# Kernel tuning notes

Hardware: AMD Instinct MI355X
Metric: run time of the kernel (lower is better)

Reference implementation:

```python
import jax, jax.numpy as jnp
import numpy as np

B, T, V, E, H = 256, 512, 30000, 256, 32


def _run_dir(x, mask, Wih, Whh, bih, bhh, reverse):
    # x: [B,T,D], mask: [B,T] bool. PyTorch GRU gate order: r, z, n.
    gi = jnp.einsum('btd,gd->btg', x, Wih) + bih  # precompute input gates [B,T,3H]
    h0 = jnp.zeros((x.shape[0], Whh.shape[1]), x.dtype)

    def step(h, inp):
        gi_t, m_t = inp
        gh = h @ Whh.T + bhh
        ir, iz, inn = jnp.split(gi_t, 3, axis=-1)
        hr, hz, hn = jnp.split(gh, 3, axis=-1)
        r = jax.nn.sigmoid(ir + hr)
        z = jax.nn.sigmoid(iz + hz)
        n = jnp.tanh(inn + r * hn)
        h_new = (1.0 - z) * n + z * h
        # packed-sequence semantics: freeze state at padded steps
        h = jnp.where(m_t[:, None], h_new, h)
        return h, h

    hT, ys = jax.lax.scan(step, h0, (jnp.swapaxes(gi, 0, 1), mask.T), reverse=reverse)
    return jnp.swapaxes(ys, 0, 1), hT  # outputs [B,T,H], final hidden [B,H]


def _bigru_layer(x, mask, pf, pb):
    of, hf = _run_dir(x, mask, *pf, reverse=False)
    ob, hb = _run_dir(x, mask, *pb, reverse=True)
    return jnp.concatenate([of, ob], axis=-1), hf, hb


def setup_inputs() -> dict:
    key = jax.random.key(0)
    ks = jax.random.split(key, 24)
    lengths = jax.random.randint(ks[0], (B,), 1, T + 1)
    mask = (jnp.arange(T)[None, :] < lengths[:, None]).astype(jnp.int32)
    ids = jax.random.randint(ks[1], (B, T), 1, V)
    ids = jnp.where(mask > 0, ids, 0)  # pad_id = 0 at padded positions
    embed = (jax.random.normal(ks[2], (V, E), jnp.float32) * 0.1).at[0].set(0.0)

    def gru_params(k, din):
        k1, k2, k3, k4 = jax.random.split(k, 4)
        s = 1.0 / np.sqrt(H)
        return (jax.random.uniform(k1, (3 * H, din), jnp.float32, -s, s),
                jax.random.uniform(k2, (3 * H, H), jnp.float32, -s, s),
                jax.random.uniform(k3, (3 * H,), jnp.float32, -s, s),
                jax.random.uniform(k4, (3 * H,), jnp.float32, -s, s))

    inp = {"input_ids": ids, "attention_mask": mask, "embed": embed}
    i = 3
    for layer, din in (("l0", E), ("l1", 2 * H)):
        for d in ("f", "b"):
            Wih, Whh, bih, bhh = gru_params(ks[i], din); i += 1
            inp[f"Wih_{layer}{d}"] = Wih
            inp[f"Whh_{layer}{d}"] = Whh
            inp[f"bih_{layer}{d}"] = bih
            inp[f"bhh_{layer}{d}"] = bhh
    s = 1.0 / np.sqrt(2 * H)
    inp["Wout"] = jax.random.uniform(ks[i], (6, 2 * H), jnp.float32, -s, s)
    inp["bout"] = jax.random.uniform(ks[i + 1], (6,), jnp.float32, -s, s)
    return inp


def reference(input_ids, attention_mask, embed,
              Wih_l0f, Whh_l0f, bih_l0f, bhh_l0f,
              Wih_l0b, Whh_l0b, bih_l0b, bhh_l0b,
              Wih_l1f, Whh_l1f, bih_l1f, bhh_l1f,
              Wih_l1b, Whh_l1b, bih_l1b, bhh_l1b,
              Wout, bout):
    mask = attention_mask > 0
    x = embed[input_ids]  # [B,T,E]
    x1, _, _ = _bigru_layer(x, mask,
                            (Wih_l0f, Whh_l0f, bih_l0f, bhh_l0f),
                            (Wih_l0b, Whh_l0b, bih_l0b, bhh_l0b))
    # no dropout: eval-mode forward
    _, hf, hb = _bigru_layer(x1, mask,
                             (Wih_l1f, Whh_l1f, bih_l1f, bhh_l1f),
                             (Wih_l1b, Whh_l1b, bih_l1b, bhh_l1b))
    top = jnp.concatenate([hf, hb], axis=-1)  # h_n[-2:] -> [B, 2H]
    return top @ Wout.T + bout  # [B, 6]
```

## Files before the change

### kernel.cpp

```cpp
#include <hip/hip_runtime.h>
#include <hip/hip_bf16.h>
#include <stdint.h>

#define B_ 256
#define T_ 512
#define V_ 30000
#define E_ 256
#define H_ 32

typedef float v2f __attribute__((ext_vector_type(2)));
typedef unsigned int uint2e __attribute__((ext_vector_type(2)));

#define LOG2E_F 1.44269504088896340736f

__device__ __forceinline__ float exp2_fast(float x) {
    float r; asm("v_exp_f32 %0, %1" : "=v"(r) : "v"(x)); return r;
}
__device__ __forceinline__ float rcp_fast(float x) {
    float r; asm("v_rcp_f32 %0, %1" : "=v"(r) : "v"(x)); return r;
}
__device__ __forceinline__ void pk_fma(v2f& acc, v2f w, v2f h) {
    asm("v_pk_fma_f32 %0, %1, %2, %0" : "+v"(acc) : "v"(w), "v"(h));
}
template <int CTRL>
__device__ __forceinline__ float mdpp(float x) {
    return __int_as_float(
        __builtin_amdgcn_mov_dpp(__float_as_int(x), CTRL, 0xF, 0xF, true));
}
#define DPP_XOR1  0xB1
#define DPP_XOR2  0x4E
#define DPP_XOR3  0x1B
#define DPP_XOR7  0x141
#define DPP_XOR15 0x140

__device__ __forceinline__ float swap32(float h) {
    uint2e r = __builtin_amdgcn_permlane32_swap(
        __float_as_uint(h), __float_as_uint(h), false, false);
    return __uint_as_float(r.x ^ r.y ^ __float_as_uint(h));
}

#define GEMM_MT 64
#define GEMM_KC 32
#define GEMM_PA 68
#define GEMM_PB 196

__global__ __launch_bounds__(256) void gemm_gates(
    const float* __restrict__ A, int M, int K,
    const float* __restrict__ Wf, const float* __restrict__ Wb,
    const float* __restrict__ bihf, const float* __restrict__ bhhf,
    const float* __restrict__ bihb, const float* __restrict__ bhhb,
    float* __restrict__ Out)
{
    __shared__ float As[GEMM_KC][GEMM_PA];
    __shared__ float Bs[GEMM_KC][GEMM_PB];

    const int tid = threadIdx.x;
    const int mbase = blockIdx.x * GEMM_MT;
    const int mg = tid >> 5, ng = tid & 31;
    const int m_off = mg * 8, n_off = ng * 6;

    float acc[8][6];
    #pragma unroll
    for (int r = 0; r < 8; ++r)
        #pragma unroll
        for (int c = 0; c < 6; ++c) acc[r][c] = 0.f;

    for (int kc = 0; kc < K; kc += GEMM_KC) {
        #pragma unroll
        for (int i = 0; i < 2; ++i) {
            int fi = tid + 256 * i;
            int row = fi >> 3, cf = fi & 7;
            int m = mbase + row;
            float4 v = make_float4(0.f, 0.f, 0.f, 0.f);
            if (m < M) v = *(const float4*)&A[(size_t)m * K + kc + cf * 4];
            As[cf * 4 + 0][row] = v.x; As[cf * 4 + 1][row] = v.y;
            As[cf * 4 + 2][row] = v.z; As[cf * 4 + 3][row] = v.w;
        }
        #pragma unroll
        for (int i = 0; i < 6; ++i) {
            int fi = tid + 256 * i;
            int g = fi >> 3, cf = fi & 7;
            const float* Wsel = (g < 96) ? (Wf + (size_t)g * K)
                                         : (Wb + (size_t)(g - 96) * K);
            float4 v = *(const float4*)&Wsel[kc + cf * 4];
            Bs[cf * 4 + 0][g] = v.x; Bs[cf * 4 + 1][g] = v.y;
            Bs[cf * 4 + 2][g] = v.z; Bs[cf * 4 + 3][g] = v.w;
        }
        __syncthreads();
        #pragma unroll
        for (int k = 0; k < GEMM_KC; ++k) {
            float a[8], bb[6];
            *(float4*)&a[0] = *(const float4*)&As[k][m_off];
            *(float4*)&a[4] = *(const float4*)&As[k][m_off + 4];
            *(float2*)&bb[0] = *(const float2*)&Bs[k][n_off];
            *(float2*)&bb[2] = *(const float2*)&Bs[k][n_off + 2];
            *(float2*)&bb[4] = *(const float2*)&Bs[k][n_off + 4];
            #pragma unroll
            for (int r = 0; r < 8; ++r)
                #pragma unroll
                for (int c = 0; c < 6; ++c)
                    acc[r][c] = fmaf(a[r], bb[c], acc[r][c]);
        }
        __syncthreads();
    }

    float bias[6], gsc[6];
    #pragma unroll
    for (int c = 0; c < 6; ++c) {
        int g = n_off + c;
        int g96 = (g < 96) ? g : g - 96;
        const float* bih = (g < 96) ? bihf : bihb;
        const float* bhh = (g < 96) ? bhhf : bhhb;
        bias[c] = bih[g96] + ((g96 < 64) ? bhh[g96] : 0.f);
        gsc[c]  = (g96 < 64) ? -LOG2E_F : 2.0f * LOG2E_F;
    }
    #pragma unroll
    for (int r = 0; r < 8; ++r) {
        int m = mbase + m_off + r;
        if (m < M) {
            float* op = &Out[(size_t)m * 192 + n_off];
            #pragma unroll
            for (int c = 0; c < 6; ++c) op[c] = (acc[r][c] + bias[c]) * gsc[c];
        }
    }
}

template <int USE_IDS>
__global__ __launch_bounds__(64, 1) void gru_scan(
    const float* __restrict__ gi,
    const int* __restrict__ ids,
    const int* __restrict__ mask,
    const float* __restrict__ Whh_f, const float* __restrict__ Whh_b,
    const float* __restrict__ bhh_f, const float* __restrict__ bhh_b,
    float* __restrict__ out_seq,
    float* __restrict__ out_fin)
{
    const int l = threadIdx.x;
    const int i16 = l & 15;
    const int row = l >> 4;
    const int hi = (row ^ (row >> 1)) & 1;
    const int j = i16 + 16 * hi;
    const bool lower = l < 32;
    const int dir = blockIdx.x & 1;
    const int b = blockIdx.x >> 1;
    const int bT = b * T_;

    const float* Whh = dir ? Whh_b : Whh_f;
    const float* bhh = dir ? bhh_b : bhh_f;

    const int kA = 16 * hi;
    const int kB = 16 - kA;

    const float sRZ = -LOG2E_F;
    const float sN2 = 2.0f * LOG2E_F;

    const int M0[8] = {0, 2, 7, 5, 15, 13, 8, 10};
    const int M1[8] = {1, 3, 6, 4, 14, 12, 9, 11};

    v2f wAR[8], wAZ[8], wAN[8], wBR[8], wBZ[8], wBN[8];
    #pragma unroll
    for (int q = 0; q < 8; ++q) {
        const int a0 = kA + (i16 ^ M0[q]);
        const int a1 = kA + (i16 ^ M1[q]);
        const int b0 = kB + (i16 ^ M0[q]);
        const int b1 = kB + (i16 ^ M1[q]);
        wAR[q] = (v2f){Whh[j * 32 + a0] * sRZ, Whh[j * 32 + a1] * sRZ};
        wAZ[q] = (v2f){Whh[(32 + j) * 32 + a0] * sRZ, Whh[(32 + j) * 32 + a1] * sRZ};
        wAN[q] = (v2f){Whh[(64 + j) * 32 + a0] * sN2, Whh[(64 + j) * 32 + a1] * sN2};
        wBR[q] = (v2f){Whh[j * 32 + b0] * sRZ, Whh[j * 32 + b1] * sRZ};
        wBZ[q] = (v2f){Whh[(32 + j) * 32 + b0] * sRZ, Whh[(32 + j) * 32 + b1] * sRZ};
        wBN[q] = (v2f){Whh[(64 + j) * 32 + b0] * sN2, Whh[(64 + j) * 32 + b1] * sN2};
    }
    float bns = bhh[64 + j] * sN2;

    #pragma unroll
    for (int q = 0; q < 8; ++q) {
        asm volatile("" : "+v"(wAR[q]), "+v"(wAZ[q]), "+v"(wAN[q]),
                          "+v"(wBR[q]), "+v"(wBZ[q]), "+v"(wBN[q]));
    }
    asm volatile("" : "+v"(bns));

    const int offR = dir * 96 + j;
    const int offZ = dir * 96 + 32 + j;
    const int offN = dir * 96 + 64 + j;

    auto wbase = [&](int c) { return dir ? (bT + 508 - 4 * c) : (bT + 4 * c); };

    int4 ids0 = make_int4(0, 0, 0, 0);
    if (USE_IDS) ids0 = *(const int4*)&ids[wbase(0)];
    int4 mask_use = *(const int4*)&mask[wbase(0)];
    int4 mask_mid = *(const int4*)&mask[wbase(1)];
    int4 mask_in  = make_int4(0, 0, 0, 0);
    int4 ids_pf = make_int4(0, 0, 0, 0), ids_mid = ids_pf, ids_in = ids_pf;
    if (USE_IDS) {
        ids_pf  = *(const int4*)&ids[wbase(1)];
        ids_mid = *(const int4*)&ids[wbase(2)];
    }

    float gR[2][4], gZ[2][4], gN[2][4];
    #pragma unroll
    for (int u = 0; u < 4; ++u) {
        int rowi;
        if (USE_IDS) {
            const int* ip = (const int*)&ids0;
            rowi = dir ? ip[3 - u] : ip[u];
        } else {
            rowi = bT + (dir ? (511 - u) : u);
        }
        const float* gp = gi + (size_t)rowi * 192;
        gR[0][u] = gp[offR];
        gZ[0][u] = gp[offZ];
        gN[0][u] = gp[offN];
    }

    float h = 0.f;

    for (int c2 = 0; c2 < 64; ++c2) {
        #pragma unroll
        for (int pb = 0; pb < 2; ++pb) {
            const int c = 2 * c2 + pb;
            if (USE_IDS) {
                const int ci = (c + 3 < 128) ? (c + 3) : 127;
                ids_in = *(const int4*)&ids[wbase(ci)];
            }
            {
                const int cm = (c + 2 < 128) ? (c + 2) : 127;
                mask_in = *(const int4*)&mask[wbase(cm)];
            }
            const int cN = (c + 1 < 128) ? (c + 1) : 127;

            #pragma unroll
            for (int u = 0; u < 4; ++u) {
                int rowN;
                if (USE_IDS) {
                    const int* ip = (const int*)&ids_pf;
                    rowN = dir ? ip[3 - u] : ip[u];
                } else {
                    rowN = bT + (dir ? (511 - 4 * cN - u) : (4 * cN + u));
                }
                const float* gpN = gi + (size_t)rowN * 192;
                gR[pb ^ 1][u] = gpN[offR];
                gZ[pb ^ 1][u] = gpN[offZ];
                gN[pb ^ 1][u] = gpN[offN];

                const int* mu = (const int*)&mask_use;
                const int m = dir ? mu[3 - u] : mu[u];

                const float hs = swap32(h);

                v2f p[8], p2[8];
                {
                    p[0].x = h;                       p[0].y = mdpp<DPP_XOR1>(h);
                    p[1].x = mdpp<DPP_XOR2>(h);       p[1].y = mdpp<DPP_XOR3>(h);
                    p[2].x = mdpp<DPP_XOR7>(h);       p[2].y = mdpp<DPP_XOR7>(p[0].y);
                    p[3].x = mdpp<DPP_XOR7>(p[1].x);  p[3].y = mdpp<DPP_XOR7>(p[1].y);
                    p[4].x = mdpp<DPP_XOR15>(h);      p[4].y = mdpp<DPP_XOR15>(p[0].y);
                    p[5].x = mdpp<DPP_XOR15>(p[1].x); p[5].y = mdpp<DPP_XOR15>(p[1].y);
                    p[6].x = mdpp<DPP_XOR15>(p[2].x); p[6].y = mdpp<DPP_XOR15>(p[2].y);
                    p[7].x = mdpp<DPP_XOR15>(p[3].x); p[7].y = mdpp<DPP_XOR15>(p[3].y);

                    p2[0].x = hs;                       p2[0].y = mdpp<DPP_XOR1>(hs);
                    p2[1].x = mdpp<DPP_XOR2>(hs);       p2[1].y = mdpp<DPP_XOR3>(hs);
                    p2[2].x = mdpp<DPP_XOR7>(hs);       p2[2].y = mdpp<DPP_XOR7>(p2[0].y);
                    p2[3].x = mdpp<DPP_XOR7>(p2[1].x);  p2[3].y = mdpp<DPP_XOR7>(p2[1].y);
                    p2[4].x = mdpp<DPP_XOR15>(hs);      p2[4].y = mdpp<DPP_XOR15>(p2[0].y);
                    p2[5].x = mdpp<DPP_XOR15>(p2[1].x); p2[5].y = mdpp<DPP_XOR15>(p2[1].y);
                    p2[6].x = mdpp<DPP_XOR15>(p2[2].x); p2[6].y = mdpp<DPP_XOR15>(p2[2].y);
                    p2[7].x = mdpp<DPP_XOR15>(p2[3].x); p2[7].y = mdpp<DPP_XOR15>(p2[3].y);
                }

                v2f aR0 = {0.f, 0.f}, aZ0 = {0.f, 0.f}, aN0 = {0.f, 0.f};
                v2f aR1 = {0.f, 0.f}, aZ1 = {0.f, 0.f}, aN1 = {0.f, 0.f};
                #pragma unroll
                for (int q = 0; q < 8; ++q) {
                    pk_fma(aR0, wAR[q], p[q]);
                    pk_fma(aZ0, wAZ[q], p[q]);
                    pk_fma(aN0, wAN[q], p[q]);
                    pk_fma(aR1, wBR[q], p2[q]);
                    pk_fma(aZ1, wBZ[q], p2[q]);
                    pk_fma(aN1, wBN[q], p2[q]);
                }
                const v2f sR = aR0 + aR1;
                const v2f sZ = aZ0 + aZ1;
                const v2f sN = aN0 + aN1;

                const float yr  = (gR[pb][u] + sR.x) + sR.y;
                const float yz  = (gZ[pb][u] + sZ.x) + sZ.y;
                const float hns = (bns + sN.x) + sN.y;
                const float r = rcp_fast(1.0f + exp2_fast(yr));
                const float z = rcp_fast(1.0f + exp2_fast(yz));
                const float yn = gN[pb][u] + r * hns;
                const float n = fmaf(-2.0f, rcp_fast(1.0f + exp2_fast(yn)), 1.0f);
                const float hnew = n + z * (h - n);
                h = m ? hnew : h;

                if (out_seq != nullptr) {
                    const int t = dir ? (511 - 4 * c - u) : (4 * c + u);
                    if (lower)
                        out_seq[(size_t)(bT + t) * 64 + dir * 32 + j] = h;
                }
            }
            mask_use = mask_mid; mask_mid = mask_in;
            if (USE_IDS) { ids_pf = ids_mid; ids_mid = ids_in; }
        }
    }

    if (out_fin != nullptr && lower)
        out_fin[b * 64 + dir * 32 + j] = h;
}

__global__ void head_kernel(const float* __restrict__ hfin,
                            const float* __restrict__ Wout,
                            const float* __restrict__ bout,
                            float* __restrict__ out)
{
    int idx = blockIdx.x * blockDim.x + threadIdx.x;
    if (idx >= B_ * 6) return;
    int b = idx / 6, o = idx % 6;
    float acc = bout[o];
    const float* hp = hfin + b * 64;
    const float* wp = Wout + o * 64;
    #pragma unroll
    for (int k = 0; k < 64; ++k) acc = fmaf(hp[k], wp[k], acc);
    out[idx] = acc;
}

extern "C" void kernel_launch(void* const* d_in, const int* in_sizes, int n_in,
                              void* d_out, int out_size, void* d_ws, size_t ws_size,
                              hipStream_t stream)
{
    const int*   ids   = (const int*)d_in[0];
    const int*   mask  = (const int*)d_in[1];
    const float* embed = (const float*)d_in[2];
    const float* Wih0f = (const float*)d_in[3];
    const float* Whh0f = (const float*)d_in[4];
    const float* bih0f = (const float*)d_in[5];
    const float* bhh0f = (const float*)d_in[6];
    const float* Wih0b = (const float*)d_in[7];
    const float* Whh0b = (const float*)d_in[8];
    const float* bih0b = (const float*)d_in[9];
    const float* bhh0b = (const float*)d_in[10];
    const float* Wih1f = (const float*)d_in[11];
    const float* Whh1f = (const float*)d_in[12];
    const float* bih1f = (const float*)d_in[13];
    const float* bhh1f = (const float*)d_in[14];
    const float* Wih1b = (const float*)d_in[15];
    const float* Whh1b = (const float*)d_in[16];
    const float* bih1b = (const float*)d_in[17];
    const float* bhh1b = (const float*)d_in[18];
    const float* Wout  = (const float*)d_in[19];
    const float* bout  = (const float*)d_in[20];

    float* ws   = (float*)d_ws;
    float* gbuf = ws;
    float* x1   = ws + (size_t)B_ * T_ * 192;
    float* hfin = x1 + (size_t)B_ * T_ * 64;

    gemm_gates<<<(V_ + GEMM_MT - 1) / GEMM_MT, 256, 0, stream>>>(
        embed, V_, E_, Wih0f, Wih0b, bih0f, bhh0f, bih0b, bhh0b, gbuf);

    gru_scan<1><<<2 * B_, 64, 0, stream>>>(
        gbuf, ids, mask, Whh0f, Whh0b, bhh0f, bhh0b, x1, nullptr);

    gemm_gates<<<(B_ * T_) / GEMM_MT, 256, 0, stream>>>(
        x1, B_ * T_, 64, Wih1f, Wih1b, bih1f, bhh1f, bih1b, bhh1b, gbuf);

    gru_scan<0><<<2 * B_, 64, 0, stream>>>(
        gbuf, nullptr, mask, Whh1f, Whh1b, bhh1f, bhh1b, nullptr, hfin);

    head_kernel<<<(B_ * 6 + 255) / 256, 256, 0, stream>>>(hfin, Wout, bout,
                                                          (float*)d_out);
}
```

Before: 525.4 us.

## Split GRU recurrent matvec across wave halves and reduce partial sums via permlane32

Result: faster. 482.4 us (-8.2%).

```diff
diff --git a/kernel.cpp b/kernel.cpp
--- a/kernel.cpp
+++ b/kernel.cpp
@@ -33,10 +33,15 @@
 #define DPP_XOR7  0x141
 #define DPP_XOR15 0x140
 
-__device__ __forceinline__ float swap32(float h) {
+__device__ __forceinline__ float swap32(float x) {
     uint2e r = __builtin_amdgcn_permlane32_swap(
-        __float_as_uint(h), __float_as_uint(h), false, false);
-    return __uint_as_float(r.x ^ r.y ^ __float_as_uint(h));
+        __float_as_uint(x), __float_as_uint(x), false, false);
+    return __uint_as_float(r.x ^ r.y ^ __float_as_uint(x));
+}
+__device__ __forceinline__ float swap16(float x) {
+    uint2e r = __builtin_amdgcn_permlane16_swap(
+        __float_as_uint(x), __float_as_uint(x), false, false);
+    return __uint_as_float(r.x ^ r.y ^ __float_as_uint(x));
 }
 
 #define GEMM_MT 64
@@ -126,7 +131,9 @@
 }
 
 template <int USE_IDS>
-__global__ __launch_bounds__(64, 1) void gru_scan(
+__global__ __launch_bounds__(64, 1)
+__attribute__((amdgpu_waves_per_eu(1, 1)))
+void gru_scan(
     const float* __restrict__ gi,
     const int* __restrict__ ids,
     const int* __restrict__ mask,
@@ -138,9 +145,11 @@
     const int l = threadIdx.x;
     const int i16 = l & 15;
     const int row = l >> 4;
-    const int hi = (row ^ (row >> 1)) & 1;
+    const int hi = row & 1;
+    const int kh = row >> 1;
     const int j = i16 + 16 * hi;
     const bool lower = l < 32;
+    const bool self_seed = (hi == kh);
     const int dir = blockIdx.x & 1;
     const int b = blockIdx.x >> 1;
     const int bT = b * T_;
@@ -148,36 +157,28 @@
     const float* Whh = dir ? Whh_b : Whh_f;
     const float* bhh = dir ? bhh_b : bhh_f;
 
-    const int kA = 16 * hi;
-    const int kB = 16 - kA;
-
     const float sRZ = -LOG2E_F;
     const float sN2 = 2.0f * LOG2E_F;
 
     const int M0[8] = {0, 2, 7, 5, 15, 13, 8, 10};
     const int M1[8] = {1, 3, 6, 4, 14, 12, 9, 11};
 
-    v2f wAR[8], wAZ[8], wAN[8], wBR[8], wBZ[8], wBN[8];
+    v2f wR[8], wZ[8], wN[8];
     #pragma unroll
     for (int q = 0; q < 8; ++q) {
-        const int a0 = kA + (i16 ^ M0[q]);
-        const int a1 = kA + (i16 ^ M1[q]);
-        const int b0 = kB + (i16 ^ M0[q]);
-        const int b1 = kB + (i16 ^ M1[q]);
-        wAR[q] = (v2f){Whh[j * 32 + a0] * sRZ, Whh[j * 32 + a1] * sRZ};
-        wAZ[q] = (v2f){Whh[(32 + j) * 32 + a0] * sRZ, Whh[(32 + j) * 32 + a1] * sRZ};
-        wAN[q] = (v2f){Whh[(64 + j) * 32 + a0] * sN2, Whh[(64 + j) * 32 + a1] * sN2};
-        wBR[q] = (v2f){Whh[j * 32 + b0] * sRZ, Whh[j * 32 + b1] * sRZ};
-        wBZ[q] = (v2f){Whh[(32 + j) * 32 + b0] * sRZ, Whh[(32 + j) * 32 + b1] * sRZ};
-        wBN[q] = (v2f){Whh[(64 + j) * 32 + b0] * sN2, Whh[(64 + j) * 32 + b1] * sN2};
+        const int c0 = kh * 16 + (i16 ^ M0[q]);
+        const int c1 = kh * 16 + (i16 ^ M1[q]);
+        wR[q] = (v2f){Whh[j * 32 + c0] * sRZ, Whh[j * 32 + c1] * sRZ};
+        wZ[q] = (v2f){Whh[(32 + j) * 32 + c0] * sRZ,
+                      Whh[(32 + j) * 32 + c1] * sRZ};
+        wN[q] = (v2f){Whh[(64 + j) * 32 + c0] * sN2,
+                      Whh[(64 + j) * 32 + c1] * sN2};
     }
     float bns = bhh[64 + j] * sN2;
 
     #pragma unroll
-    for (int q = 0; q < 8; ++q) {
-        asm volatile("" : "+v"(wAR[q]), "+v"(wAZ[q]), "+v"(wAN[q]),
-                          "+v"(wBR[q]), "+v"(wBZ[q]), "+v"(wBN[q]));
-    }
+    for (int q = 0; q < 8; ++q)
+        asm volatile("" : "+v"(wR[q]), "+v"(wZ[q]), "+v"(wN[q]));
     asm volatile("" : "+v"(bns));
 
     const int offR = dir * 96 + j;
@@ -246,47 +247,36 @@
                 const int* mu = (const int*)&mask_use;
                 const int m = dir ? mu[3 - u] : mu[u];
 
-                const float hs = swap32(h);
-
-                v2f p[8], p2[8];
-                {
-                    p[0].x = h;                       p[0].y = mdpp<DPP_XOR1>(h);
-                    p[1].x = mdpp<DPP_XOR2>(h);       p[1].y = mdpp<DPP_XOR3>(h);
-                    p[2].x = mdpp<DPP_XOR7>(h);       p[2].y = mdpp<DPP_XOR7>(p[0].y);
-                    p[3].x = mdpp<DPP_XOR7>(p[1].x);  p[3].y = mdpp<DPP_XOR7>(p[1].y);
-                    p[4].x = mdpp<DPP_XOR15>(h);      p[4].y = mdpp<DPP_XOR15>(p[0].y);
-                    p[5].x = mdpp<DPP_XOR15>(p[1].x); p[5].y = mdpp<DPP_XOR15>(p[1].y);
-                    p[6].x = mdpp<DPP_XOR15>(p[2].x); p[6].y = mdpp<DPP_XOR15>(p[2].y);
-                    p[7].x = mdpp<DPP_XOR15>(p[3].x); p[7].y = mdpp<DPP_XOR15>(p[3].y);
-
-                    p2[0].x = hs;                       p2[0].y = mdpp<DPP_XOR1>(hs);
-                    p2[1].x = mdpp<DPP_XOR2>(hs);       p2[1].y = mdpp<DPP_XOR3>(hs);
-                    p2[2].x = mdpp<DPP_XOR7>(hs);       p2[2].y = mdpp<DPP_XOR7>(p2[0].y);
-                    p2[3].x = mdpp<DPP_XOR7>(p2[1].x);  p2[3].y = mdpp<DPP_XOR7>(p2[1].y);
-                    p2[4].x = mdpp<DPP_XOR15>(hs);      p2[4].y = mdpp<DPP_XOR15>(p2[0].y);
-                    p2[5].x = mdpp<DPP_XOR15>(p2[1].x); p2[5].y = mdpp<DPP_XOR15>(p2[1].y);
-                    p2[6].x = mdpp<DPP_XOR15>(p2[2].x); p2[6].y = mdpp<DPP_XOR15>(p2[2].y);
-                    p2[7].x = mdpp<DPP_XOR15>(p2[3].x); p2[7].y = mdpp<DPP_XOR15>(p2[3].y);
-                }
-
-                v2f aR0 = {0.f, 0.f}, aZ0 = {0.f, 0.f}, aN0 = {0.f, 0.f};
-                v2f aR1 = {0.f, 0.f}, aZ1 = {0.f, 0.f}, aN1 = {0.f, 0.f};
+                const float hx = swap16(h);
+                const float seed = self_seed ? h : hx;
+
+                v2f p[8];
+                p[0].x = seed;                      p[0].y = mdpp<DPP_XOR1>(seed);
+                p[1].x = mdpp<DPP_XOR2>(seed);      p[1].y = mdpp<DPP_XOR3>(seed);
+                p[2].x = mdpp<DPP_XOR7>(seed);      p[2].y = mdpp<DPP_XOR7>(p[0].y);
+                p[3].x = mdpp<DPP_XOR7>(p[1].x);    p[3].y = mdpp<DPP_XOR7>(p[1].y);
+                p[4].x = mdpp<DPP_XOR15>(seed);     p[4].y = mdpp<DPP_XOR15>(p[0].y);
+                p[5].x = mdpp<DPP_XOR15>(p[1].x);   p[5].y = mdpp<DPP_XOR15>(p[1].y);
+                p[6].x = mdpp<DPP_XOR15>(p[2].x);   p[6].y = mdpp<DPP_XOR15>(p[2].y);
+                p[7].x = mdpp<DPP_XOR15>(p[3].x);   p[7].y = mdpp<DPP_XOR15>(p[3].y);
+
+                v2f aR = {0.f, 0.f}, aZ = {0.f, 0.f}, aN = {0.f, 0.f};
                 #pragma unroll
                 for (int q = 0; q < 8; ++q) {
-                    pk_fma(aR0, wAR[q], p[q]);
-                    pk_fma(aZ0, wAZ[q], p[q]);
-                    pk_fma(aN0, wAN[q], p[q]);
-                    pk_fma(aR1, wBR[q], p2[q]);
-                    pk_fma(aZ1, wBZ[q], p2[q]);
-                    pk_fma(aN1, wBN[q], p2[q]);
+                    pk_fma(aR, wR[q], p[q]);
+                    pk_fma(aZ, wZ[q], p[q]);
+                    pk_fma(aN, wN[q], p[q]);
                 }
-                const v2f sR = aR0 + aR1;
-                const v2f sZ = aZ0 + aZ1;
-                const v2f sN = aN0 + aN1;
-
-                const float yr  = (gR[pb][u] + sR.x) + sR.y;
-                const float yz  = (gZ[pb][u] + sZ.x) + sZ.y;
-                const float hns = (bns + sN.x) + sN.y;
+                const float sR = aR.x + aR.y;
+                const float sZ = aZ.x + aZ.y;
+                const float sN = aN.x + aN.y;
+                const float SR = sR + swap32(sR);
+                const float SZ = sZ + swap32(sZ);
+                const float SN = sN + swap32(sN);
+
+                const float yr  = gR[pb][u] + SR;
+                const float yz  = gZ[pb][u] + SZ;
+                const float hns = bns + SN;
                 const float r = rcp_fast(1.0f + exp2_fast(yr));
                 const float z = rcp_fast(1.0f + exp2_fast(yz));
                 const float yn = gN[pb][u] + r * hns;
```
